# Kernel tuning notes

Hardware: AMD Instinct MI355X
Metric: run time of the kernel (lower is better)

Reference implementation:

```python
import jax, jax.numpy as jnp
import numpy as np

B, Hg, Wg, K, D, SD = 4, 128, 128, 16, 256, 64
N = Hg * Wg
MGAT_R0 = 1.5
TV_W = 1e-3
BIG_NEG = -10000.0
LN_EPS = 1e-5
# (r, s0, sl, cb) per geodesic scale
SCALES = ((1.5, 0.25, 0.2, 0.7), (2.5, 0.35, 0.2, 0.5), (4.0, 0.55, 0.25, 0.3))


def _build_grid_knn(H, W, Kn):
    # K nearest grid offsets (incl. self), deterministic tie-break
    cand = [(dy, dx) for dy in range(-3, 4) for dx in range(-3, 4)]
    cand.sort(key=lambda o: (o[0] * o[0] + o[1] * o[1], o[0], o[1]))
    offs = np.array(cand[:Kn])                                  # (K,2)
    ii, jj = np.meshgrid(np.arange(H), np.arange(W), indexing='ij')
    pos = np.stack([ii.ravel(), jj.ravel()], -1)                # (N,2)
    nb = pos[:, None, :] + offs[None]                           # (N,K,2)
    nb[..., 0] = np.clip(nb[..., 0], 0, H - 1)
    nb[..., 1] = np.clip(nb[..., 1], 0, W - 1)
    idx = (nb[..., 0] * W + nb[..., 1]).astype(np.int32)        # (N,K)
    rel = (nb - pos[:, None, :]).astype(np.float32)             # (N,K,2)
    geod = np.sqrt((rel ** 2).sum(-1)).astype(np.float32)       # (N,K)
    rel = rel / np.clip(np.abs(rel).max(axis=(0, 1), keepdims=True), 1e-6, None)
    return idx, rel, geod


def _lin(key, fan_in, fan_out):
    kw, kb = jax.random.split(key)
    s = 1.0 / np.sqrt(fan_in)
    return (jax.random.uniform(kw, (fan_in, fan_out), jnp.float32, -s, s),
            jax.random.uniform(kb, (fan_out,), jnp.float32, -s, s))


def setup_inputs() -> dict:
    key = jax.random.key(0)
    ks = jax.random.split(key, 14)
    idx, rel, geod = _build_grid_knn(Hg, Wg, K)
    inp = {
        'z': jax.random.normal(ks[0], (B, N, D), jnp.float32),
        'S': jax.random.normal(ks[1], (B, N, SD), jnp.float32),
        'rel': jnp.asarray(rel), 'geod': jnp.asarray(geod), 'idx': jnp.asarray(idx),
    }
    inp['Wq'], inp['bq'] = _lin(ks[2], D, D)
    inp['Wk'], inp['bk'] = _lin(ks[3], D, D)
    inp['Wv'], inp['bv'] = _lin(ks[4], D, D)
    inp['Wo'], inp['bo'] = _lin(ks[5], D, D)
    inp['ln_g'] = jnp.ones((D,), jnp.float32)
    inp['ln_b'] = jnp.zeros((D,), jnp.float32)
    inp['Ws1'], inp['bs1'] = _lin(ks[6], 2, 16)
    inp['Ws2'], inp['bs2'] = _lin(ks[7], 16, 16)
    inp['Wzg'], inp['bzg'] = _lin(ks[8], D, 16)
    inp['Wph'], inp['bph'] = _lin(ks[9], 32, 3)
    inp['Wsg'], inp['bsg'] = _lin(ks[10], 32, 3)
    return inp


def _forward(z, S, rel, geod, Wq, bq, Wk, bk, Wv, bv, Wo, bo, ln_g, ln_b,
             Ws1, bs1, Ws2, bs2, Wzg, bzg, Wph, bph, Wsg, bsg, idx):
    gelu = lambda x: jax.nn.gelu(x, approximate=False)
    q = z @ Wq + bq
    k = z @ Wk + bk
    v = z @ Wv + bv
    kN = k[:, idx]                                   # (B,N,K,D) neighbor gather
    vN = v[:, idx]                                   # (B,N,K,D)
    S_n = S[:, idx]                                  # (B,N,K,SD)
    m1 = S.mean(-1, keepdims=True)
    m2 = (S * S).mean(-1, keepdims=True)
    s_emb = gelu(gelu(jnp.concatenate([m1, m2], -1) @ Ws1 + bs1) @ Ws2 + bs2)
    z_emb = gelu(z @ Wzg + bzg)
    ker_in = jnp.concatenate([s_emb, z_emb], -1)     # (B,N,32)
    abc = ker_in @ Wph + bph                         # (B,N,3)
    La = jnp.exp(abc[..., 0]); Lb = abc[..., 1]; Lc = jnp.exp(abc[..., 2])
    # A = L L^T with L = [[La,0],[Lb,Lc]] -> symmetric 2x2 per node
    A00 = La * La; A01 = La * Lb; A11 = Lb * Lb + Lc * Lc   # (B,N)
    r0 = rel[None, ..., 0]; r1 = rel[None, ..., 1]          # (1,N,K)
    rAr = (A00[..., None] * r0 * r0 + 2.0 * A01[..., None] * r0 * r1
           + A11[..., None] * r1 * r1)                      # (B,N,K)
    sim = jnp.einsum('bns,bnks->bnk', S, S_n)
    content = jnp.einsum('bnd,bnkd->bnk', q, kN) / np.sqrt(D).astype(np.float32)
    g = jax.nn.softmax(ker_in @ Wsg + bsg, axis=-1)         # (B,N,3)
    geod_b = geod[None]                                     # (1,N,K)
    center_prior = jnp.exp(-geod_b ** 2 / MGAT_R0 ** 2)
    att_logits = jnp.zeros_like(content)
    for i, (r, s0, sl, cb) in enumerate(SCALES):
        hard_mask = (geod > r).astype(z.dtype)[None]
        sigma2 = jnp.maximum((s0 + sl * geod_b) ** 2, 1e-6)
        att_i = (content - rAr / sigma2 - 0.25 * geod_b + 1.0 * sim
                 + cb * center_prior + hard_mask * BIG_NEG)
        att_logits = att_logits + att_i * g[..., i:i + 1]
    att = jax.nn.softmax(att_logits, axis=-1)               # (B,N,K)
    agg = jnp.einsum('bnk,bnkd->bnd', att, vN)
    h = z + (agg @ Wo + bo)                                 # dropout/drop_path = identity (eval)
    mu = h.mean(-1, keepdims=True)
    var = ((h - mu) ** 2).mean(-1, keepdims=True)
    out = ln_g * (h - mu) / jnp.sqrt(var + LN_EPS) + ln_b
    # TV regularizer on Frobenius norm of A over the HxW grid
    A_norm = jnp.sqrt(A00 * A00 + 2.0 * A01 * A01 + A11 * A11).reshape(B, Hg, Wg)
    dy = jnp.abs(A_norm[:, 1:, :] - A_norm[:, :-1, :]).mean()
    dx = jnp.abs(A_norm[:, :, 1:] - A_norm[:, :, :-1]).mean()
    reg = TV_W * (dx + dy)
    return out, reg


def reference(z, S, rel, geod, idx, Wq, bq, Wk, bk, Wv, bv, Wo, bo, ln_g, ln_b,
              Ws1, bs1, Ws2, bs2, Wzg, bzg, Wph, bph, Wsg, bsg):
    return _forward(z, S, rel, geod, Wq, bq, Wk, bk, Wv, bv, Wo, bo, ln_g, ln_b,
                    Ws1, bs1, Ws2, bs2, Wzg, bzg, Wph, bph, Wsg, bsg, idx)
```

## Files before the change

kernel.cpp:

```cpp
#include <hip/hip_runtime.h>
#include <hip/hip_bf16.h>
#include <math.h>


typedef unsigned short u16;
typedef unsigned int u32;
typedef __attribute__((ext_vector_type(8))) short short8;
typedef __attribute__((ext_vector_type(4))) float f32x4;

#define NB 16384
#define NROWS 65536
#define DD 256
#define SDD 64

__device__ __forceinline__ float b2f(u16 u) {
  union { unsigned int i; float f; } c; c.i = ((unsigned int)u) << 16; return c.f;
}
__device__ __forceinline__ float blo(unsigned int u) {
  union { unsigned int i; float f; } c; c.i = u << 16; return c.f;
}
__device__ __forceinline__ float bhi(unsigned int u) {
  union { unsigned int i; float f; } c; c.i = u & 0xFFFF0000u; return c.f;
}
__device__ __forceinline__ u16 f2b(float f) {
  union { float f; unsigned int i; } c; c.f = f;
  unsigned int i = c.i;
  return (u16)((i + 0x7FFFu + ((i >> 16) & 1u)) >> 16);
}
__device__ __forceinline__ float gelu_exact(float x) {
  return 0.5f * x * (1.0f + erff(x * 0.70710678118654752f));
}
__device__ __forceinline__ void gll16(const u16* g, u16* l) {
  __builtin_amdgcn_global_load_lds(
      (const __attribute__((address_space(1))) void*)g,
      (__attribute__((address_space(3))) void*)l, 16, 0, 0);
}
__device__ __forceinline__ u32 qsc(u32 w) {
  float lo = __uint_as_float(w << 16) * 0.0625f;
  float hi = __uint_as_float(w & 0xFFFF0000u) * 0.0625f;
  return (__float_as_uint(lo) >> 16) | (__float_as_uint(hi) & 0xFFFF0000u);
}

__global__ __launch_bounds__(256) void k_prep_w(
    const float* __restrict__ Wq, const float* __restrict__ Wk,
    const float* __restrict__ Wv, const float* __restrict__ Wo,
    const float* __restrict__ Wzg,
    const float* __restrict__ bq, const float* __restrict__ bk,
    const float* __restrict__ bv, const float* __restrict__ bzg,
    u16* __restrict__ WqkvT, u16* __restrict__ WoT, float* __restrict__ biasq)
{
  int gid = blockIdx.x * 256 + threadIdx.x;
  int stride = gridDim.x * 256;
  for (int e = gid; e < 229376; e += stride) {
    int j = e >> 8, kk = e & 255;
    float v;
    if (j < 256)      v = Wq[kk * 256 + j];
    else if (j < 512) v = Wk[kk * 256 + (j - 256)];
    else if (j < 768) v = Wv[kk * 256 + (j - 512)];
    else if (j < 784) v = Wzg[kk * 16 + (j - 768)];
    else              v = 0.0f;
    WqkvT[e] = f2b(v);
  }
  for (int e = gid; e < 65536; e += stride) {
    int j = e >> 8, kk = e & 255;
    WoT[e] = f2b(Wo[kk * 256 + j]);
  }
  for (int e = gid; e < 784; e += stride)
    biasq[e] = e < 256 ? bq[e] : e < 512 ? bk[e - 256]
             : e < 768 ? bv[e - 512] : bzg[e - 768];
}

__global__ __launch_bounds__(256) void k_pre(
    const float* __restrict__ z, const float* __restrict__ S,
    u16* __restrict__ zb, float* __restrict__ rowdat)
{
  int w = threadIdx.x >> 6, t = threadIdx.x & 63;
  int r = blockIdx.x * 4 + w;
  float4 zv = *(const float4*)(z + (size_t)r * DD + t * 4);
  *(ushort4*)(zb + (size_t)r * DD + t * 4) =
      make_ushort4(f2b(zv.x), f2b(zv.y), f2b(zv.z), f2b(zv.w));
  float sv = S[(size_t)r * SDD + t];
  float s1 = sv, s2 = sv * sv;
  #pragma unroll
  for (int o = 32; o; o >>= 1) { s1 += __shfl_xor(s1, o); s2 += __shfl_xor(s2, o); }
  if (t == 0) {
    rowdat[(size_t)r * 8 + 0] = s1 * (1.0f / 64.0f);
    rowdat[(size_t)r * 8 + 1] = s2 * (1.0f / 64.0f);
  }
}

__global__ __launch_bounds__(256) void k_mfma_qkv(
    const u16* __restrict__ A, const u16* __restrict__ BT,
    const float* __restrict__ biasq,
    u16* __restrict__ qb, u16* __restrict__ kb, u16* __restrict__ vb,
    float* __restrict__ ze)
{
  __shared__ u16 As[128 * 64];
  __shared__ u16 Bs[128 * 64];
  int t = threadIdx.x, wv = t >> 6, lane = t & 63;
  int m0 = blockIdx.x * 128, j0 = blockIdx.y * 128;
  int wm = (wv & 1) * 64, wn = (wv >> 1) * 64;
  int quad = lane >> 4, l15 = lane & 15;
  int x7 = l15 & 7;
  int srow = lane >> 3;
  int scolsw = ((lane & 7) ^ (srow & 7)) << 3;
  f32x4 acc[4][4] = {};
  for (int kc = 0; kc < 256; kc += 64) {
    if (kc) __syncthreads();
    for (int it = 0; it < 4; ++it) {
      int c = it * 4 + wv;
      gll16(A + (size_t)(m0 + c * 8 + srow) * 256 + kc + scolsw, As + c * 512);
      gll16(BT + (size_t)(j0 + c * 8 + srow) * 256 + kc + scolsw, Bs + c * 512);
    }
    __syncthreads();
    #pragma unroll
    for (int ks = 0; ks < 64; ks += 32) {
      short8 af[4], bfr[4];
      int sl = (ks >> 3) + quad;
      #pragma unroll
      for (int mi = 0; mi < 4; ++mi)
        af[mi] = *(const short8*)&As[(wm + mi * 16 + l15) * 64 + ((sl ^ x7) << 3)];
      #pragma unroll
      for (int ni = 0; ni < 4; ++ni)
        bfr[ni] = *(const short8*)&Bs[(wn + ni * 16 + l15) * 64 + ((sl ^ x7) << 3)];
      #pragma unroll
      for (int mi = 0; mi < 4; ++mi)
        #pragma unroll
        for (int ni = 0; ni < 4; ++ni)
          acc[mi][ni] = __builtin_amdgcn_mfma_f32_16x16x32_bf16(
              af[mi], bfr[ni], acc[mi][ni], 0, 0, 0);
    }
  }
  if (j0 < 768) {
    u16* obuf = (j0 < 256) ? qb : (j0 < 512) ? kb : vb;
    int jb = j0 & 255;
    #pragma unroll
    for (int ni = 0; ni < 4; ++ni) {
      int gcol = j0 + wn + ni * 16 + l15;
      float bia = biasq[gcol];
      int colb = jb + wn + ni * 16 + l15;
      #pragma unroll
      for (int mi = 0; mi < 4; ++mi) {
        int grow = m0 + wm + mi * 16 + quad * 4;
        #pragma unroll
        for (int r = 0; r < 4; ++r)
          obuf[(size_t)(grow + r) * 256 + colb] = f2b(acc[mi][ni][r] + bia);
      }
    }
  } else if (wn == 0) {
    float bia = biasq[768 + l15];
    #pragma unroll
    for (int mi = 0; mi < 4; ++mi) {
      int grow = m0 + wm + mi * 16 + quad * 4;
      #pragma unroll
      for (int r = 0; r < 4; ++r)
        ze[(size_t)(grow + r) * 16 + l15] = gelu_exact(acc[mi][0][r] + bia);
    }
  }
}

__global__ __launch_bounds__(256) void k_post(
    const float* __restrict__ ze,
    const float* __restrict__ Ws1, const float* __restrict__ bs1,
    const float* __restrict__ Ws2, const float* __restrict__ bs2,
    const float* __restrict__ Wph, const float* __restrict__ bph,
    const float* __restrict__ Wsg, const float* __restrict__ bsg,
    float* __restrict__ rowdat)
{
  __shared__ float h1s[16][17];
  __shared__ float kin[16][33];
  __shared__ float abcs[16][8];
  int rloc = threadIdx.x >> 4, j = threadIdx.x & 15;
  int r = blockIdx.x * 16 + rloc;
  float m1 = rowdat[(size_t)r * 8 + 0];
  float m2 = rowdat[(size_t)r * 8 + 1];
  h1s[rloc][j] = gelu_exact(m1 * Ws1[j] + m2 * Ws1[16 + j] + bs1[j]);
  __syncthreads();
  float h2 = bs2[j];
  #pragma unroll
  for (int i = 0; i < 16; ++i) h2 += h1s[rloc][i] * Ws2[i * 16 + j];
  kin[rloc][j] = gelu_exact(h2);
  kin[rloc][16 + j] = ze[(size_t)r * 16 + j];
  __syncthreads();
  if (j < 6) {
    int c = j % 3;
    const float* Wp = (j < 3) ? Wph : Wsg;
    const float* bp = (j < 3) ? bph : bsg;
    float a = bp[c];
    #pragma unroll
    for (int i = 0; i < 32; ++i) a += kin[rloc][i] * Wp[i * 3 + c];
    abcs[rloc][j] = a;
  }
  __syncthreads();
  if (j == 0) {
    float La = expf(abcs[rloc][0]), Lb = abcs[rloc][1], Lc = expf(abcs[rloc][2]);
    float A00 = La * La, A01 = La * Lb, A11 = Lb * Lb + Lc * Lc;
    float g0 = abcs[rloc][3], g1 = abcs[rloc][4], g2 = abcs[rloc][5];
    float gm = fmaxf(g0, fmaxf(g1, g2));
    float e0 = expf(g0 - gm), e1 = expf(g1 - gm), e2 = expf(g2 - gm);
    float inv = 1.0f / (e0 + e1 + e2);
    float* rd = rowdat + (size_t)r * 8;
    rd[0] = A00; rd[1] = A01; rd[2] = A11;
    rd[3] = e0 * inv; rd[4] = e1 * inv; rd[5] = e2 * inv;
    rd[6] = sqrtf(A00 * A00 + 2.0f * A01 * A01 + A11 * A11);
  }
}

#define DYP 0x1004220331132212ULL
#define DXP 0x0312402313123122ULL

__global__ __launch_bounds__(256) void k_attn_mfma(
    const u16* __restrict__ q, const u16* __restrict__ k,
    const u16* __restrict__ v, const float* __restrict__ S,
    const float* __restrict__ rowdat, u16* __restrict__ aggp)
{
  __shared__ u16 KV[18432];
  __shared__ u16 Qs[16 * 264];
  __shared__ u16 Shi[64 * 72];
  __shared__ u16 Slo[64 * 72];
  __shared__ float scores[16 * 68];
  __shared__ float attf[16 * 68];
  __shared__ u16 attb[16 * 72];
  __shared__ float rds[16 * 8];

  int tid = threadIdx.x;
  int bid = blockIdx.x;
  int gidx = (bid & 7) * 512 + (bid >> 3);
  int b = gidx >> 10;
  int gid = gidx & 1023;
  int gy0 = (gid >> 5) << 2, gx0 = (gid & 31) << 2;
  int by0 = gy0 - 2; by0 = by0 < 0 ? 0 : (by0 > 120 ? 120 : by0);
  int bx0 = gx0 - 2; bx0 = bx0 < 0 ? 0 : (bx0 > 120 ? 120 : bx0);
  int oy = gy0 - by0, ox = gx0 - bx0;
  size_t bbase = (size_t)b << 14;

  int vpp = tid & 31, vdc = tid >> 5;
  size_t vn0 = bbase + (size_t)(by0 + (vpp >> 2)) * 128 + bx0 + ((vpp & 3) * 2);
  const u16* v0 = v + vn0 * 256;
  uint4 va[4], vb4[4];
  #pragma unroll
  for (int i = 0; i < 4; ++i) {
    va[i]  = *(const uint4*)(v0 + (vdc + i * 8) * 8);
    vb4[i] = *(const uint4*)(v0 + 256 + (vdc + i * 8) * 8);
  }

  {
    int rr8 = tid >> 5, cc = tid & 31;
    #pragma unroll
    for (int p = 0; p < 8; ++p) {
      size_t n = bbase + (size_t)(by0 + p) * 128 + bx0 + rr8;
      uint4 ld = *(const uint4*)(k + n * 256 + cc * 8);
      *(uint4*)&KV[(p * 8 + rr8) * 264 + cc * 8] = ld;
    }
    #pragma unroll
    for (int p = 0; p < 2; ++p) {
      int r = p * 8 + rr8;
      size_t n = bbase + (size_t)(gy0 + (r >> 2)) * 128 + gx0 + (r & 3);
      uint4 ld = *(const uint4*)(q + n * 256 + cc * 8);
      uint4 o;
      o.x = qsc(ld.x); o.y = qsc(ld.y); o.z = qsc(ld.z); o.w = qsc(ld.w);
      *(uint4*)&Qs[r * 264 + cc * 8] = o;
    }
  }
  {
    int u = tid >> 2, qq = tid & 3;
    size_t n = bbase + (size_t)(by0 + (u >> 3)) * 128 + bx0 + (u & 7);
    const float* srow = S + n * 64 + qq * 16;
    u32 hw[8], lw[8];
    #pragma unroll
    for (int i = 0; i < 4; ++i) {
      float4 s4 = *(const float4*)(srow + i * 4);
      u32 bx_ = __float_as_uint(s4.x), by_ = __float_as_uint(s4.y);
      u32 bz_ = __float_as_uint(s4.z), bw_ = __float_as_uint(s4.w);
      u32 hx = bx_ & 0xFFFF0000u, hy = by_ & 0xFFFF0000u;
      u32 hz = bz_ & 0xFFFF0000u, hww = bw_ & 0xFFFF0000u;
      hw[i * 2]     = (bx_ >> 16) | hy;
      hw[i * 2 + 1] = (bz_ >> 16) | hww;
      lw[i * 2]     = (__float_as_uint(s4.x - __uint_as_float(hx)) >> 16)
                    | (__float_as_uint(s4.y - __uint_as_float(hy)) & 0xFFFF0000u);
      lw[i * 2 + 1] = (__float_as_uint(s4.z - __uint_as_float(hz)) >> 16)
                    | (__float_as_uint(s4.w - __uint_as_float(hww)) & 0xFFFF0000u);
    }
    *(uint4*)&Shi[u * 72 + qq * 16]     = make_uint4(hw[0], hw[1], hw[2], hw[3]);
    *(uint4*)&Shi[u * 72 + qq * 16 + 8] = make_uint4(hw[4], hw[5], hw[6], hw[7]);
    *(uint4*)&Slo[u * 72 + qq * 16]     = make_uint4(lw[0], lw[1], lw[2], lw[3]);
    *(uint4*)&Slo[u * 72 + qq * 16 + 8] = make_uint4(lw[4], lw[5], lw[6], lw[7]);
  }
  if (tid < 128) {
    int r = tid >> 3, sl = tid & 7;
    size_t n = bbase + (size_t)(gy0 + (r >> 2)) * 128 + gx0 + (r & 3);
    rds[tid] = rowdat[n * 8 + sl];
  }
  for (int i = tid; i < 16 * 68; i += 256) attf[i] = 0.0f;
  __syncthreads();

  int w = tid >> 6, lane = tid & 63, l15 = lane & 15, quad = lane >> 4;

  {
    f32x4 acc = {0.f, 0.f, 0.f, 0.f};
    int arow = l15 * 264 + quad * 8;
    int brow = (w * 16 + l15) * 264 + quad * 8;
    #pragma unroll
    for (int ks = 0; ks < 8; ++ks) {
      short8 a  = *(const short8*)&Qs[arow + ks * 32];
      short8 bq = *(const short8*)&KV[brow + ks * 32];
      acc = __builtin_amdgcn_mfma_f32_16x16x32_bf16(a, bq, acc, 0, 0, 0);
    }
    int ucq = ((l15 >> 2) + oy) * 8 + (l15 & 3) + ox;
    int sa = ucq * 72 + quad * 8;
    int sb = (w * 16 + l15) * 72 + quad * 8;
    #pragma unroll
    for (int ks = 0; ks < 2; ++ks) {
      short8 ah = *(const short8*)&Shi[sa + ks * 32];
      short8 al = *(const short8*)&Slo[sa + ks * 32];
      short8 bh = *(const short8*)&Shi[sb + ks * 32];
      short8 bl = *(const short8*)&Slo[sb + ks * 32];
      acc = __builtin_amdgcn_mfma_f32_16x16x32_bf16(ah, bh, acc, 0, 0, 0);
      acc = __builtin_amdgcn_mfma_f32_16x16x32_bf16(ah, bl, acc, 0, 0, 0);
      acc = __builtin_amdgcn_mfma_f32_16x16x32_bf16(al, bh, acc, 0, 0, 0);
    }
    #pragma unroll
    for (int r4 = 0; r4 < 4; ++r4)
      scores[(quad * 4 + r4) * 68 + w * 16 + l15] = acc[r4];
  }
  __syncthreads();

  {
    int r = tid >> 4, g = tid & 15;
    int gy = gy0 + (r >> 2), gx = gx0 + (r & 3);
    int dy = (int)((DYP >> (g * 4)) & 15) - 2;
    int dx = (int)((DXP >> (g * 4)) & 15) - 2;
    int ny = gy + dy; ny = ny < 0 ? 0 : (ny > 127 ? 127 : ny);
    int nx = gx + dx; nx = nx < 0 ? 0 : (nx > 127 ? 127 : nx);
    int cdy = ny - gy, cdx = nx - gx;
    int u = (ny - by0) * 8 + (nx - bx0);
    float sc = scores[r * 68 + u];
    const float* rd = &rds[r * 8];
    float A00 = rd[0], A01 = rd[1], A11 = rd[2];
    float g0 = rd[3], g1 = rd[4], g2 = rd[5];
    float r0 = cdy * 0.5f, r1 = cdx * 0.5f;
    int ig2 = cdy * cdy + cdx * cdx;
    float ge2 = (float)ig2;
    float ge = sqrtf(ge2);
    float rAr = A00 * r0 * r0 + 2.0f * A01 * r0 * r1 + A11 * r1 * r1;
    float prior = __expf(-ge2 * (1.0f / 2.25f));
    float lg = sc - 0.25f * ge;
    { float s = 0.25f + 0.2f  * ge; float s2 = fmaxf(s * s, 1e-6f);
      lg += g0 * (-rAr * __builtin_amdgcn_rcpf(s2) + 0.7f * prior
                  + (ig2 >= 3  ? -10000.0f : 0.0f)); }
    { float s = 0.35f + 0.2f  * ge; float s2 = fmaxf(s * s, 1e-6f);
      lg += g1 * (-rAr * __builtin_amdgcn_rcpf(s2) + 0.5f * prior
                  + (ig2 >= 7  ? -10000.0f : 0.0f)); }
    { float s = 0.55f + 0.25f * ge; float s2 = fmaxf(s * s, 1e-6f);
      lg += g2 * (-rAr * __builtin_amdgcn_rcpf(s2) + 0.3f * prior
                  + (ig2 >= 17 ? -10000.0f : 0.0f)); }
    float m = lg;
    m = fmaxf(m, __shfl_xor(m, 1));
    m = fmaxf(m, __shfl_xor(m, 2));
    m = fmaxf(m, __shfl_xor(m, 4));
    m = fmaxf(m, __shfl_xor(m, 8));
    float e = __expf(lg - m);
    float sm = e;
    sm += __shfl_xor(sm, 1); sm += __shfl_xor(sm, 2);
    sm += __shfl_xor(sm, 4); sm += __shfl_xor(sm, 8);
    float att = e * __builtin_amdgcn_rcpf(sm);
    atomicAdd(&attf[r * 68 + u], att);
  }
  __syncthreads();

  {
    int r = tid >> 4, c4 = (tid & 15) * 4;
    float4 fv = *(const float4*)&attf[r * 68 + c4];
    u32 w0 = (u32)f2b(fv.x) | ((u32)f2b(fv.y) << 16);
    u32 w1 = (u32)f2b(fv.z) | ((u32)f2b(fv.w) << 16);
    *(uint2*)&attb[r * 72 + c4] = make_uint2(w0, w1);
  }
  {
    u32* VTw = (u32*)KV;
    #pragma unroll
    for (int i = 0; i < 4; ++i) {
      int d0 = (vdc + i * 8) * 8;
      u32 a0 = va[i].x, a1 = va[i].y, a2 = va[i].z, a3 = va[i].w;
      u32 b0 = vb4[i].x, b1 = vb4[i].y, b2 = vb4[i].z, b3 = vb4[i].w;
      VTw[(d0 + 0) * 36 + vpp] = (a0 & 0xFFFFu) | (b0 << 16);
      VTw[(d0 + 1) * 36 + vpp] = (a0 >> 16)     | (b0 & 0xFFFF0000u);
      VTw[(d0 + 2) * 36 + vpp] = (a1 & 0xFFFFu) | (b1 << 16);
      VTw[(d0 + 3) * 36 + vpp] = (a1 >> 16)     | (b1 & 0xFFFF0000u);
      VTw[(d0 + 4) * 36 + vpp] = (a2 & 0xFFFFu) | (b2 << 16);
      VTw[(d0 + 5) * 36 + vpp] = (a2 >> 16)     | (b2 & 0xFFFF0000u);
      VTw[(d0 + 6) * 36 + vpp] = (a3 & 0xFFFFu) | (b3 << 16);
      VTw[(d0 + 7) * 36 + vpp] = (a3 >> 16)     | (b3 & 0xFFFF0000u);
    }
  }
  __syncthreads();

  {
    short8 a0 = *(const short8*)&attb[l15 * 72 + quad * 8];
    short8 a1 = *(const short8*)&attb[l15 * 72 + 32 + quad * 8];
    #pragma unroll
    for (int ni = 0; ni < 4; ++ni) {
      int d = w * 64 + ni * 16 + l15;
      f32x4 ag = {0.f, 0.f, 0.f, 0.f};
      short8 bv0 = *(const short8*)&KV[d * 72 + quad * 8];
      short8 bv1 = *(const short8*)&KV[d * 72 + 32 + quad * 8];
      ag = __builtin_amdgcn_mfma_f32_16x16x32_bf16(a0, bv0, ag, 0, 0, 0);
      ag = __builtin_amdgcn_mfma_f32_16x16x32_bf16(a1, bv1, ag, 0, 0, 0);
      #pragma unroll
      for (int r4 = 0; r4 < 4; ++r4) {
        int row = quad * 4 + r4;
        size_t n = bbase + (size_t)(gy0 + (row >> 2)) * 128 + gx0 + (row & 3);
        aggp[n * 256 + d] = f2b(ag[r4]);
      }
    }
  }
}

__global__ __launch_bounds__(256) void k_mfma_out_ln(
    const u16* __restrict__ A, const u16* __restrict__ BT,
    const float* __restrict__ bo, const float* __restrict__ zres,
    const float* __restrict__ lng, const float* __restrict__ lnb,
    float* __restrict__ outp)
{
  __shared__ u16 As[128 * 64];
  __shared__ u16 Bs[256 * 64];
  int t = threadIdx.x, wv = t >> 6, lane = t & 63;
  int m0 = blockIdx.x * 128;
  int wm = wv * 32;
  int quad = lane >> 4, l15 = lane & 15;
  int x7 = l15 & 7;
  int srow = lane >> 3;
  int scolsw = ((lane & 7) ^ (srow & 7)) << 3;
  f32x4 acc[2][16] = {};
  for (int kc = 0; kc < 256; kc += 64) {
    if (kc) __syncthreads();
    #pragma unroll
    for (int it = 0; it < 4; ++it) {
      int c = it * 4 + wv;
      gll16(A + (size_t)(m0 + c * 8 + srow) * 256 + kc + scolsw, As + c * 512);
    }
    #pragma unroll
    for (int it = 0; it < 8; ++it) {
      int c = it * 4 + wv;
      gll16(BT + (size_t)(c * 8 + srow) * 256 + kc + scolsw, Bs + c * 512);
    }
    __syncthreads();
    #pragma unroll
    for (int ks = 0; ks < 64; ks += 32) {
      short8 af[2], bfr[16];
      int sl = (ks >> 3) + quad;
      #pragma unroll
      for (int mi = 0; mi < 2; ++mi)
        af[mi] = *(const short8*)&As[(wm + mi * 16 + l15) * 64 + ((sl ^ x7) << 3)];
      #pragma unroll
      for (int ni = 0; ni < 16; ++ni)
        bfr[ni] = *(const short8*)&Bs[(ni * 16 + l15) * 64 + ((sl ^ x7) << 3)];
      #pragma unroll
      for (int mi = 0; mi < 2; ++mi)
        #pragma unroll
        for (int ni = 0; ni < 16; ++ni)
          acc[mi][ni] = __builtin_amdgcn_mfma_f32_16x16x32_bf16(
              af[mi], bfr[ni], acc[mi][ni], 0, 0, 0);
    }
  }
  float lg_[16], lb_[16], bo_[16];
  #pragma unroll
  for (int ni = 0; ni < 16; ++ni) {
    int col = ni * 16 + l15;
    lg_[ni] = lng[col]; lb_[ni] = lnb[col]; bo_[ni] = bo[col];
  }
  #pragma unroll
  for (int mi = 0; mi < 2; ++mi) {
    #pragma unroll
    for (int rr = 0; rr < 4; ++rr) {
      int row = m0 + wm + mi * 16 + quad * 4 + rr;
      float x[16];
      float s = 0.0f, sq = 0.0f;
      #pragma unroll
      for (int ni = 0; ni < 16; ++ni) {
        int col = ni * 16 + l15;
        float v = acc[mi][ni][rr] + bo_[ni] + zres[(size_t)row * 256 + col];
        x[ni] = v; s += v; sq += v * v;
      }
      #pragma unroll
      for (int o = 1; o < 16; o <<= 1) {
        s += __shfl_xor(s, o);
        sq += __shfl_xor(sq, o);
      }
      float mu = s * (1.0f / 256.0f);
      float var = sq * (1.0f / 256.0f) - mu * mu;
      float rstd = rsqrtf(var + 1e-5f);
      #pragma unroll
      for (int ni = 0; ni < 16; ++ni) {
        int col = ni * 16 + l15;
        outp[(size_t)row * 256 + col] = lg_[ni] * (x[ni] - mu) * rstd + lb_[ni];
      }
    }
  }
}

__global__ __launch_bounds__(256) void k_tv(
    const float* __restrict__ rowdat, float* __restrict__ sums)
{
  int gid = blockIdx.x * blockDim.x + threadIdx.x;
  int stride = gridDim.x * blockDim.x;
  float dy = 0.0f, dx = 0.0f;
  for (int e = gid; e < 4 * 127 * 128; e += stride) {
    int bb = e / 16256; int rem = e % 16256;
    int i = rem >> 7; int jj = rem & 127;
    int base = bb * 16384 + i * 128 + jj;
    dy += fabsf(rowdat[(size_t)(base + 128) * 8 + 6] - rowdat[(size_t)base * 8 + 6]);
  }
  for (int e = gid; e < 4 * 128 * 127; e += stride) {
    int bb = e / 16256; int rem = e % 16256;
    int i = rem / 127; int jj = rem % 127;
    int base = bb * 16384 + i * 128 + jj;
    dx += fabsf(rowdat[(size_t)(base + 1) * 8 + 6] - rowdat[(size_t)base * 8 + 6]);
  }
  #pragma unroll
  for (int o = 32; o; o >>= 1) { dy += __shfl_down(dy, o); dx += __shfl_down(dx, o); }
  if ((threadIdx.x & 63) == 0) {
    atomicAdd(&sums[0], dy);
    atomicAdd(&sums[1], dx);
  }
}

__global__ void k_reg(const float* __restrict__ sums, float* __restrict__ out)
{
  if (threadIdx.x == 0 && blockIdx.x == 0) {
    out[16777216] = 0.001f * (sums[0] + sums[1]) * (1.0f / 65024.0f);
  }
}

extern "C" void kernel_launch(void* const* d_in, const int* in_sizes, int n_in,
                              void* d_out, int out_size, void* d_ws, size_t ws_size,
                              hipStream_t stream)
{
  const float* z    = (const float*)d_in[0];
  const float* S    = (const float*)d_in[1];
  const float* rel  = (const float*)d_in[2];
  const float* geod = (const float*)d_in[3];
  const int*   idx  = (const int*)d_in[4];
  const float* Wq = (const float*)d_in[5];  const float* bq = (const float*)d_in[6];
  const float* Wk = (const float*)d_in[7];  const float* bk = (const float*)d_in[8];
  const float* Wv = (const float*)d_in[9];  const float* bv = (const float*)d_in[10];
  const float* Wo = (const float*)d_in[11]; const float* bo = (const float*)d_in[12];
  const float* lng = (const float*)d_in[13]; const float* lnb = (const float*)d_in[14];
  const float* Ws1 = (const float*)d_in[15]; const float* bs1 = (const float*)d_in[16];
  const float* Ws2 = (const float*)d_in[17]; const float* bs2 = (const float*)d_in[18];
  const float* Wzg = (const float*)d_in[19]; const float* bzg = (const float*)d_in[20];
  const float* Wph = (const float*)d_in[21]; const float* bph = (const float*)d_in[22];
  const float* Wsg = (const float*)d_in[23]; const float* bsg = (const float*)d_in[24];
  (void)rel; (void)geod; (void)idx;

  char* ws = (char*)d_ws;
  u16* zb = (u16*)ws;  ws += 33554432;
  u16* qb = (u16*)ws;  ws += 33554432;
  u16* kb = (u16*)ws;  ws += 33554432;
  u16* vb = (u16*)ws;  ws += 33554432;
  u16* WqkvT = (u16*)ws; ws += 458752;
  u16* WoT   = (u16*)ws; ws += 131072;
  float* biasq = (float*)ws; ws += 3136;
  float* ze    = (float*)ws; ws += 4194304;
  float* rowdat = (float*)ws; ws += 2097152;
  float* sums   = (float*)ws;
  u16* ab = zb;

  float* outp = (float*)d_out;

  hipMemsetAsync(sums, 0, 8, stream);
  k_prep_w<<<256, 256, 0, stream>>>(Wq, Wk, Wv, Wo, Wzg, bq, bk, bv, bzg,
                                    WqkvT, WoT, biasq);
  k_pre<<<NROWS / 4, 256, 0, stream>>>(z, S, zb, rowdat);
  k_mfma_qkv<<<dim3(512, 7), 256, 0, stream>>>(zb, WqkvT, biasq, qb, kb, vb, ze);
  k_post<<<NROWS / 16, 256, 0, stream>>>(ze, Ws1, bs1, Ws2, bs2,
                                         Wph, bph, Wsg, bsg, rowdat);
  k_attn_mfma<<<4096, 256, 0, stream>>>(qb, kb, vb, S, rowdat, ab);
  k_mfma_out_ln<<<512, 256, 0, stream>>>(ab, WoT, bo, z, lng, lnb, outp);
  k_tv<<<256, 256, 0, stream>>>(rowdat, sums);
  k_reg<<<1, 64, 0, stream>>>(sums, outp);
}
```

Measured before the change: 381.8 us.

## Stage QKV GEMM epilogue through LDS and remap blocks per XCD

The QKV GEMM epilogue now writes bf16 results into shared memory first, then emits coalesced 16-byte row stores instead of scattered 2-byte strided stores. The grid is flattened to 1D and remapped so the 7 column tiles of the same row tile land on the same XCD, which lets them share the A tile in L2. This adds two barriers and reuses the A/B LDS buffers. The remap relies on the round-robin block-to-XCD dispatch order of the hardware.

```diff
diff --git a/kernel.cpp b/kernel.cpp
--- a/kernel.cpp
+++ b/kernel.cpp
@@ -95,10 +95,14 @@
     u16* __restrict__ qb, u16* __restrict__ kb, u16* __restrict__ vb,
     float* __restrict__ ze)
 {
-  __shared__ u16 As[128 * 64];
-  __shared__ u16 Bs[128 * 64];
+  __shared__ u16 sm[16384];
+  u16* As = sm;
+  u16* Bs = sm + 8192;
   int t = threadIdx.x, wv = t >> 6, lane = t & 63;
-  int m0 = blockIdx.x * 128, j0 = blockIdx.y * 128;
+  int bid = blockIdx.x;
+  int xcd = bid & 7, slot = bid >> 3;
+  int mt = xcd * 64 + slot / 7, jt = slot % 7;
+  int m0 = mt * 128, j0 = jt * 128;
   int wm = (wv & 1) * 64, wn = (wv >> 1) * 64;
   int quad = lane >> 4, l15 = lane & 15;
   int x7 = l15 & 7;
@@ -132,20 +136,28 @@
     }
   }
   if (j0 < 768) {
+    __syncthreads();
+    #pragma unroll
+    for (int ni = 0; ni < 4; ++ni) {
+      int col = wn + ni * 16 + l15;
+      float bia = biasq[j0 + col];
+      #pragma unroll
+      for (int mi = 0; mi < 4; ++mi) {
+        int row = wm + mi * 16 + quad * 4;
+        #pragma unroll
+        for (int r = 0; r < 4; ++r)
+          sm[(row + r) * 128 + col] = f2b(acc[mi][ni][r] + bia);
+      }
+    }
+    __syncthreads();
     u16* obuf = (j0 < 256) ? qb : (j0 < 512) ? kb : vb;
     int jb = j0 & 255;
     #pragma unroll
-    for (int ni = 0; ni < 4; ++ni) {
-      int gcol = j0 + wn + ni * 16 + l15;
-      float bia = biasq[gcol];
-      int colb = jb + wn + ni * 16 + l15;
-      #pragma unroll
-      for (int mi = 0; mi < 4; ++mi) {
-        int grow = m0 + wm + mi * 16 + quad * 4;
-        #pragma unroll
-        for (int r = 0; r < 4; ++r)
-          obuf[(size_t)(grow + r) * 256 + colb] = f2b(acc[mi][ni][r] + bia);
-      }
+    for (int it = 0; it < 8; ++it) {
+      int e = it * 256 + t;
+      int lrow = e >> 4, cc8 = (e & 15) * 8;
+      uint4 val = *(const uint4*)&sm[lrow * 128 + cc8];
+      *(uint4*)(obuf + (size_t)(m0 + lrow) * 256 + jb + cc8) = val;
     }
   } else if (wn == 0) {
     float bia = biasq[768 + l15];
@@ -571,7 +583,7 @@
   k_prep_w<<<256, 256, 0, stream>>>(Wq, Wk, Wv, Wo, Wzg, bq, bk, bv, bzg,
                                     WqkvT, WoT, biasq);
   k_pre<<<NROWS / 4, 256, 0, stream>>>(z, S, zb, rowdat);
-  k_mfma_qkv<<<dim3(512, 7), 256, 0, stream>>>(zb, WqkvT, biasq, qb, kb, vb, ze);
+  k_mfma_qkv<<<3584, 256, 0, stream>>>(zb, WqkvT, biasq, qb, kb, vb, ze);
   k_post<<<NROWS / 16, 256, 0, stream>>>(ze, Ws1, bs1, Ws2, bs2,
                                          Wph, bph, Wsg, bsg, rowdat);
   k_attn_mfma<<<4096, 256, 0, stream>>>(qb, kb, vb, S, rowdat, ab);
```

Result: faster. 363.2 us (-4.9%).
